# Kernel tuning notes

Hardware: AMD Instinct MI355X
Metric: run time of the kernel (lower is better)

## Reference

```python
import jax, jax.numpy as jnp
import numpy as np

EPS = 1e-8

def setup_inputs() -> dict:
    key = jax.random.key(0)
    k1, k2, k3, k4 = jax.random.split(key, 4)
    B, S, K, N = 8, 32, 8192, 8192
    x = jax.random.normal(k1, (B, S, K), dtype=jnp.float32)
    # unpacked AWQ 4-bit weights: int8 values in [-8, 7] (stored as int32 here)
    qweight = jax.random.randint(k2, (K, N), -8, 8, dtype=jnp.int32)
    w_scales = jax.random.uniform(k3, (N,), dtype=jnp.float32) * 0.01 + 1e-4
    bias = jax.random.normal(k4, (N,), dtype=jnp.float32)
    return {"x": x, "qweight": qweight, "w_scales": w_scales, "bias": bias}

def reference(x, qweight, w_scales, bias):
    K = x.shape[-1]
    x2 = x.reshape(-1, K)                                  # [M, K]
    # per-token symmetric int8 activation quantization
    max_abs = jnp.max(jnp.abs(x2), axis=-1, keepdims=True)  # [M, 1]
    act_scales = jnp.maximum(max_abs / 127.0, EPS)
    x_q = jnp.clip(jnp.round(x2 / act_scales), -127, 127).astype(jnp.int8)
    out = x_q.astype(jnp.float32) @ qweight.astype(jnp.float32)  # [M, N]
    # dequant rescale: per-token * per-channel, then bias
    out = out * act_scales * w_scales[None, :] + bias[None, :]
    out = out.reshape(*x.shape[:-1], out.shape[-1])
    return out.astype(x.dtype)
```

## Files before the change

kernel.cpp:

```cpp
#include <hip/hip_runtime.h>

#define M_ 256
#define K_ 8192
#define N_ 8192

typedef int v4i __attribute__((ext_vector_type(4)));
typedef int v16i __attribute__((ext_vector_type(16)));

__global__ __launch_bounds__(256) void awq_quant(const float* __restrict__ x,
                                                 signed char* __restrict__ xqt,
                                                 float* __restrict__ scales) {
    const int m = blockIdx.x;
    const int t = threadIdx.x;
    const float4* xrow = (const float4*)(x + (size_t)m * K_);
    float4 v[8];
    float mx = 0.0f;
#pragma unroll
    for (int j = 0; j < 8; ++j) {
        v[j] = xrow[j * 256 + t];
        mx = fmaxf(mx, fmaxf(fmaxf(fabsf(v[j].x), fabsf(v[j].y)),
                             fmaxf(fabsf(v[j].z), fabsf(v[j].w))));
    }
#pragma unroll
    for (int off = 32; off > 0; off >>= 1) mx = fmaxf(mx, __shfl_xor(mx, off, 64));
    __shared__ float red[4];
    if ((t & 63) == 0) red[t >> 6] = mx;
    __syncthreads();
    mx = fmaxf(fmaxf(red[0], red[1]), fmaxf(red[2], red[3]));
    const float scale = fmaxf(mx / 127.0f, 1e-8f);

    char* base = (char*)xqt + ((size_t)(m >> 5) << 18);
    const int ml = m & 31;
#pragma unroll
    for (int j = 0; j < 8; ++j) {
        const int q0 = (int)fminf(fmaxf(rintf(v[j].x / scale), -127.0f), 127.0f);
        const int q1 = (int)fminf(fmaxf(rintf(v[j].y / scale), -127.0f), 127.0f);
        const int q2 = (int)fminf(fmaxf(rintf(v[j].z / scale), -127.0f), 127.0f);
        const int q3 = (int)fminf(fmaxf(rintf(v[j].w / scale), -127.0f), 127.0f);
        const int packed = (q0 & 255) | ((q1 & 255) << 8) | ((q2 & 255) << 16) | ((q3 & 255) << 24);
        const int k0 = 4 * (j * 256 + t);
        const int addr = ((k0 >> 8) << 13) + (((k0 >> 5) & 7) << 10) +
                         ((ml + (((k0 >> 4) & 1) << 5)) << 4) + (k0 & 15);
        *(int*)(base + addr) = packed;
    }
    if (t == 0) scales[m] = scale;
}


__device__ __forceinline__ void stage_b(char* btn, int bwo,
                                        const int4& w0, const int4& w1,
                                        const int4& w2, const int4& w3) {
    const int* p0 = (const int*)&w0;
    const int* p1 = (const int*)&w1;
    const int* p2 = (const int*)&w2;
    const int* p3 = (const int*)&w3;
#pragma unroll
    for (int j = 0; j < 4; ++j) {
        const unsigned u = __builtin_amdgcn_perm((unsigned)p1[j], (unsigned)p0[j], 0x00000400u);
        const unsigned w = __builtin_amdgcn_perm((unsigned)p3[j], (unsigned)p2[j], 0x00000400u);
        const unsigned o = __builtin_amdgcn_perm(w, u, 0x05040100u);
        *(unsigned*)(btn + bwo + j * 272) = o;
    }
}

__global__ __launch_bounds__(512) void awq_gemm(const signed char* __restrict__ xqt,
                                                const float* __restrict__ scales,
                                                const int* __restrict__ qw,
                                                const float* __restrict__ wscale,
                                                const float* __restrict__ bias,
                                                float* __restrict__ out) {
    __shared__ __align__(16) char btile[2][32 * 272];
    const int t = threadIdx.x;
    const int lane = t & 63;
    const int wave = t >> 6;
    const int n0 = blockIdx.x * 32;

    const int sa = t & 7;
    const int sr = t >> 3;
    const int* qbase = qw + (size_t)(4 * sr) * N_ + n0 + 4 * sa;

    const signed char* xqb = xqt + ((size_t)wave << 18) + lane * 16;

    const int bro = (lane & 31) * 272 + (lane >> 5) * 16;
    const int bwo = (4 * sa) * 272 + 4 * sr;

    v16i acc = {};
    v4i aF[8];
    int4 sA[4], sB[4];

    auto loadq = [&](int4* dst, int chunk) {
        const int4* q = (const int4*)(qbase + (size_t)chunk * 256 * N_);
        dst[0] = q[0];
        dst[1] = q[N_ / 4];
        dst[2] = q[2 * (N_ / 4)];
        dst[3] = q[3 * (N_ / 4)];
    };

    loadq(sA, 0);
    loadq(sB, 1);
#pragma unroll
    for (int ks = 0; ks < 8; ++ks) aF[ks] = *(const v4i*)(xqb + ks * 1024);
    stage_b(&btile[0][0], bwo, sA[0], sA[1], sA[2], sA[3]);
    asm volatile("s_waitcnt lgkmcnt(0)" ::: "memory");
    __builtin_amdgcn_s_barrier();
    __builtin_amdgcn_sched_barrier(0);

    for (int sc = 0; sc < 32; sc += 2) {
        {
            const int c2 = (sc + 2 < 32) ? sc + 2 : 31;
            loadq(sA, c2);
            const int an = (sc + 1 < 32) ? sc + 1 : 31;
            const char* btc = &btile[0][0];
#pragma unroll
            for (int ks = 0; ks < 8; ++ks) {
                const v4i bf = *(const v4i*)(btc + bro + ks * 32);
                acc = __builtin_amdgcn_mfma_i32_32x32x32_i8(aF[ks], bf, acc, 0, 0, 0);
                aF[ks] = *(const v4i*)(xqb + an * 8192 + ks * 1024);
            }
            stage_b(&btile[1][0], bwo, sB[0], sB[1], sB[2], sB[3]);
            asm volatile("s_waitcnt lgkmcnt(0)" ::: "memory");
            __builtin_amdgcn_s_barrier();
            __builtin_amdgcn_sched_barrier(0);
        }
        {
            const int c3 = (sc + 3 < 32) ? sc + 3 : 31;
            loadq(sB, c3);
            const int an = (sc + 2 < 32) ? sc + 2 : 31;
            const char* btc = &btile[1][0];
#pragma unroll
            for (int ks = 0; ks < 8; ++ks) {
                const v4i bf = *(const v4i*)(btc + bro + ks * 32);
                acc = __builtin_amdgcn_mfma_i32_32x32x32_i8(aF[ks], bf, acc, 0, 0, 0);
                aF[ks] = *(const v4i*)(xqb + an * 8192 + ks * 1024);
            }
            stage_b(&btile[0][0], bwo, sA[0], sA[1], sA[2], sA[3]);
            asm volatile("s_waitcnt lgkmcnt(0)" ::: "memory");
            __builtin_amdgcn_s_barrier();
            __builtin_amdgcn_sched_barrier(0);
        }
    }

    const int n = n0 + (lane & 31);
    const float wn = wscale[n];
    const float bn = bias[n];
    const int mb = wave * 32 + 4 * (lane >> 5);
#pragma unroll
    for (int g = 0; g < 16; ++g) {
        const int m = mb + (g & 3) + 8 * (g >> 2);
        out[(size_t)m * N_ + n] = ((float)acc[g] * scales[m]) * wn + bn;
    }
}

extern "C" void kernel_launch(void* const* d_in, const int* in_sizes, int n_in,
                              void* d_out, int out_size, void* d_ws, size_t ws_size,
                              hipStream_t stream) {
    const float* x    = (const float*)d_in[0];
    const int*   qw   = (const int*)d_in[1];
    const float* wsc  = (const float*)d_in[2];
    const float* bias = (const float*)d_in[3];
    float* out = (float*)d_out;

    signed char* xqbuf  = (signed char*)d_ws;
    float*       scales = (float*)((char*)d_ws + (size_t)M_ * K_);

    awq_quant<<<M_, 256, 0, stream>>>(x, xqbuf, scales);
    awq_gemm<<<N_ / 32, 512, 0, stream>>>(xqbuf, scales, qw, wsc, bias, out);
}
```

Measured before the change: 66.12 us.

## Split GEMM blocks across M halves with 256 threads and 8-row weight staging

Each GEMM block now covers half of the M rows (4 waves) instead of all 256, which doubles the grid to 512 blocks of 256 threads. Each thread therefore loads 8 weight rows per chunk instead of 4 and writes 8-byte LDS stores. Block indices are ordered so that the two M-halves of each group of 8 N-tiles run adjacently, which should help the duplicated weight reads hit in L2. The intent is better occupancy and parallelism across CUs. The cost is that the int32 weights are read twice overall and each thread holds more registers.

```diff
diff --git a/kernel.cpp b/kernel.cpp
--- a/kernel.cpp
+++ b/kernel.cpp
@@ -47,60 +47,58 @@
 }
 
 
-__device__ __forceinline__ void stage_b(char* btn, int bwo,
-                                        const int4& w0, const int4& w1,
-                                        const int4& w2, const int4& w3) {
-    const int* p0 = (const int*)&w0;
-    const int* p1 = (const int*)&w1;
-    const int* p2 = (const int*)&w2;
-    const int* p3 = (const int*)&w3;
+__device__ __forceinline__ void stage_b8(char* btn, int bwo, const int4* w) {
 #pragma unroll
     for (int j = 0; j < 4; ++j) {
-        const unsigned u = __builtin_amdgcn_perm((unsigned)p1[j], (unsigned)p0[j], 0x00000400u);
-        const unsigned w = __builtin_amdgcn_perm((unsigned)p3[j], (unsigned)p2[j], 0x00000400u);
-        const unsigned o = __builtin_amdgcn_perm(w, u, 0x05040100u);
-        *(unsigned*)(btn + bwo + j * 272) = o;
+        const unsigned a0 = __builtin_amdgcn_perm((unsigned)((const int*)&w[1])[j], (unsigned)((const int*)&w[0])[j], 0x00000400u);
+        const unsigned a1 = __builtin_amdgcn_perm((unsigned)((const int*)&w[3])[j], (unsigned)((const int*)&w[2])[j], 0x00000400u);
+        const unsigned b0 = __builtin_amdgcn_perm((unsigned)((const int*)&w[5])[j], (unsigned)((const int*)&w[4])[j], 0x00000400u);
+        const unsigned b1 = __builtin_amdgcn_perm((unsigned)((const int*)&w[7])[j], (unsigned)((const int*)&w[6])[j], 0x00000400u);
+        uint2 o;
+        o.x = __builtin_amdgcn_perm(a1, a0, 0x05040100u);
+        o.y = __builtin_amdgcn_perm(b1, b0, 0x05040100u);
+        *(uint2*)(btn + bwo + j * 272) = o;
     }
 }
 
-__global__ __launch_bounds__(512) void awq_gemm(const signed char* __restrict__ xqt,
-                                                const float* __restrict__ scales,
-                                                const int* __restrict__ qw,
-                                                const float* __restrict__ wscale,
-                                                const float* __restrict__ bias,
-                                                float* __restrict__ out) {
+__global__ __launch_bounds__(256, 2) void awq_gemm(const signed char* __restrict__ xqt,
+                                                   const float* __restrict__ scales,
+                                                   const int* __restrict__ qw,
+                                                   const float* __restrict__ wscale,
+                                                   const float* __restrict__ bias,
+                                                   float* __restrict__ out) {
     __shared__ __align__(16) char btile[2][32 * 272];
     const int t = threadIdx.x;
     const int lane = t & 63;
     const int wave = t >> 6;
-    const int n0 = blockIdx.x * 32;
+    const int bid = blockIdx.x;
+    const int mhalf = (bid >> 3) & 1;
+    const int n0 = ((bid >> 4) * 8 + (bid & 7)) * 32;
 
     const int sa = t & 7;
     const int sr = t >> 3;
-    const int* qbase = qw + (size_t)(4 * sr) * N_ + n0 + 4 * sa;
+    const int* qbase = qw + (size_t)(8 * sr) * N_ + n0 + 4 * sa;
 
-    const signed char* xqb = xqt + ((size_t)wave << 18) + lane * 16;
+    const signed char* xqb = xqt + ((size_t)(mhalf * 4 + wave) << 18) + lane * 16;
 
     const int bro = (lane & 31) * 272 + (lane >> 5) * 16;
-    const int bwo = (4 * sa) * 272 + 4 * sr;
+    const int bwo = (4 * sa) * 272 + 8 * sr;
 
     v16i acc = {};
     v4i aF[8];
-    int4 sA[4], sB[4];
+    int4 sA[8], sB[8];
 
     auto loadq = [&](int4* dst, int chunk) {
         const int4* q = (const int4*)(qbase + (size_t)chunk * 256 * N_);
-        dst[0] = q[0];
-        dst[1] = q[N_ / 4];
-        dst[2] = q[2 * (N_ / 4)];
-        dst[3] = q[3 * (N_ / 4)];
+#pragma unroll
+        for (int i = 0; i < 8; ++i) dst[i] = q[i * (N_ / 4)];
     };
 
     loadq(sA, 0);
     loadq(sB, 1);
 #pragma unroll
     for (int ks = 0; ks < 8; ++ks) aF[ks] = *(const v4i*)(xqb + ks * 1024);
-    stage_b(&btile[0][0], bwo, sA[0], sA[1], sA[2], sA[3]);
+    stage_b8(&btile[0][0], bwo, sA);
     asm volatile("s_waitcnt lgkmcnt(0)" ::: "memory");
     __builtin_amdgcn_s_barrier();
     __builtin_amdgcn_sched_barrier(0);
@@ -117,7 +115,7 @@
                 acc = __builtin_amdgcn_mfma_i32_32x32x32_i8(aF[ks], bf, acc, 0, 0, 0);
                 aF[ks] = *(const v4i*)(xqb + an * 8192 + ks * 1024);
             }
-            stage_b(&btile[1][0], bwo, sB[0], sB[1], sB[2], sB[3]);
+            stage_b8(&btile[1][0], bwo, sB);
             asm volatile("s_waitcnt lgkmcnt(0)" ::: "memory");
             __builtin_amdgcn_s_barrier();
             __builtin_amdgcn_sched_barrier(0);
@@ -133,7 +131,7 @@
                 acc = __builtin_amdgcn_mfma_i32_32x32x32_i8(aF[ks], bf, acc, 0, 0, 0);
                 aF[ks] = *(const v4i*)(xqb + an * 8192 + ks * 1024);
             }
-            stage_b(&btile[0][0], bwo, sA[0], sA[1], sA[2], sA[3]);
+            stage_b8(&btile[0][0], bwo, sA);
             asm volatile("s_waitcnt lgkmcnt(0)" ::: "memory");
             __builtin_amdgcn_s_barrier();
             __builtin_amdgcn_sched_barrier(0);
@@ -143,7 +141,7 @@
     const int n = n0 + (lane & 31);
     const float wn = wscale[n];
     const float bn = bias[n];
-    const int mb = wave * 32 + 4 * (lane >> 5);
+    const int mb = (mhalf * 4 + wave) * 32 + 4 * (lane >> 5);
 #pragma unroll
     for (int g = 0; g < 16; ++g) {
         const int m = mb + (g & 3) + 8 * (g >> 2);
@@ -164,5 +162,5 @@
     float*       scales = (float*)((char*)d_ws + (size_t)M_ * K_);
 
     awq_quant<<<M_, 256, 0, stream>>>(x, xqbuf, scales);
-    awq_gemm<<<N_ / 32, 512, 0, stream>>>(xqbuf, scales, qw, wsc, bias, out);
+    awq_gemm<<<512, 256, 0, stream>>>(xqbuf, scales, qw, wsc, bias, out);
 }
```

Result: slower. 81.34 us (+23.0%).

## Deepen global-load prefetch pipeline to four stages in int8 AWQ GEMM

Applied to the files above, without the earlier changes.

Restructures the GEMM main loop from a two-deep prefetch of weights and activations to a four-deep rotating register pipeline, unrolled by four phases. Each phase issues loads for chunk+4 while computing the current chunk, so more global memory latency can be hidden. Launch bounds also request two blocks per CU, which caps registers even though the extra buffers raise register demand. That combination risks spills or lost occupancy.

```diff
diff --git a/kernel.cpp b/kernel.cpp
--- a/kernel.cpp
+++ b/kernel.cpp
@@ -63,12 +63,12 @@
     }
 }
 
-__global__ __launch_bounds__(512) void awq_gemm(const signed char* __restrict__ xqt,
-                                                const float* __restrict__ scales,
-                                                const int* __restrict__ qw,
-                                                const float* __restrict__ wscale,
-                                                const float* __restrict__ bias,
-                                                float* __restrict__ out) {
+__global__ __launch_bounds__(512, 2) void awq_gemm(const signed char* __restrict__ xqt,
+                                                   const float* __restrict__ scales,
+                                                   const int* __restrict__ qw,
+                                                   const float* __restrict__ wscale,
+                                                   const float* __restrict__ bias,
+                                                   float* __restrict__ out) {
     __shared__ __align__(16) char btile[2][32 * 272];
     const int t = threadIdx.x;
     const int lane = t & 63;
@@ -85,8 +85,8 @@
     const int bwo = (4 * sa) * 272 + 4 * sr;
 
     v16i acc = {};
-    v4i aF[8];
-    int4 sA[4], sB[4];
+    v4i a0[8], a1[8], a2[8], a3[8];
+    int4 s0[4], s1[4], s2[4], s3[4];
 
     auto loadq = [&](int4* dst, int chunk) {
         const int4* q = (const int4*)(qbase + (size_t)chunk * 256 * N_);
@@ -95,50 +95,45 @@
         dst[2] = q[2 * (N_ / 4)];
         dst[3] = q[3 * (N_ / 4)];
     };
+    auto loada = [&](v4i* a, int chunk) {
+#pragma unroll
+        for (int f = 0; f < 8; ++f)
+            a[f] = *(const v4i*)(xqb + (size_t)chunk * 8192 + f * 1024);
+    };
 
-    loadq(sA, 0);
-    loadq(sB, 1);
-#pragma unroll
-    for (int ks = 0; ks < 8; ++ks) aF[ks] = *(const v4i*)(xqb + ks * 1024);
-    stage_b(&btile[0][0], bwo, sA[0], sA[1], sA[2], sA[3]);
+    loadq(s0, 0); loada(a0, 0);
+    loadq(s1, 1); loada(a1, 1);
+    loadq(s2, 2); loada(a2, 2);
+    loadq(s3, 3); loada(a3, 3);
+    stage_b(&btile[0][0], bwo, s0[0], s0[1], s0[2], s0[3]);
     asm volatile("s_waitcnt lgkmcnt(0)" ::: "memory");
     __builtin_amdgcn_s_barrier();
     __builtin_amdgcn_sched_barrier(0);
 
-    for (int sc = 0; sc < 32; sc += 2) {
-        {
-            const int c2 = (sc + 2 < 32) ? sc + 2 : 31;
-            loadq(sA, c2);
-            const int an = (sc + 1 < 32) ? sc + 1 : 31;
-            const char* btc = &btile[0][0];
-#pragma unroll
-            for (int ks = 0; ks < 8; ++ks) {
-                const v4i bf = *(const v4i*)(btc + bro + ks * 32);
-                acc = __builtin_amdgcn_mfma_i32_32x32x32_i8(aF[ks], bf, acc, 0, 0, 0);
-                aF[ks] = *(const v4i*)(xqb + an * 8192 + ks * 1024);
-            }
-            stage_b(&btile[1][0], bwo, sB[0], sB[1], sB[2], sB[3]);
-            asm volatile("s_waitcnt lgkmcnt(0)" ::: "memory");
-            __builtin_amdgcn_s_barrier();
-            __builtin_amdgcn_sched_barrier(0);
-        }
-        {
-            const int c3 = (sc + 3 < 32) ? sc + 3 : 31;
-            loadq(sB, c3);
-            const int an = (sc + 2 < 32) ? sc + 2 : 31;
-            const char* btc = &btile[1][0];
-#pragma unroll
-            for (int ks = 0; ks < 8; ++ks) {
-                const v4i bf = *(const v4i*)(btc + bro + ks * 32);
-                acc = __builtin_amdgcn_mfma_i32_32x32x32_i8(aF[ks], bf, acc, 0, 0, 0);
-                aF[ks] = *(const v4i*)(xqb + an * 8192 + ks * 1024);
-            }
-            stage_b(&btile[0][0], bwo, sA[0], sA[1], sA[2], sA[3]);
-            asm volatile("s_waitcnt lgkmcnt(0)" ::: "memory");
-            __builtin_amdgcn_s_barrier();
-            __builtin_amdgcn_sched_barrier(0);
-        }
+#define PHASE(P_, AREG, SCUR, SNEXT, BUFC, BUFN)                                    \
+    {                                                                               \
+        const int cf = (P_) + 4;                                                    \
+        if (cf < 32) loadq(SCUR, cf);                                               \
+        const char* btc = &btile[BUFC][0];                                          \
+        _Pragma("unroll")                                                           \
+        for (int f = 0; f < 8; ++f) {                                               \
+            const v4i bf = *(const v4i*)(btc + bro + f * 32);                       \
+            acc = __builtin_amdgcn_mfma_i32_32x32x32_i8(AREG[f], bf, acc, 0, 0, 0); \
+        }                                                                           \
+        if (cf < 32) loada(AREG, cf);                                               \
+        stage_b(&btile[BUFN][0], bwo, SNEXT[0], SNEXT[1], SNEXT[2], SNEXT[3]);      \
+        asm volatile("s_waitcnt lgkmcnt(0)" ::: "memory");                          \
+        __builtin_amdgcn_s_barrier();                                               \
+        __builtin_amdgcn_sched_barrier(0);                                          \
     }
+
+    for (int sc = 0; sc < 32; sc += 4) {
+        PHASE(sc + 0, a0, s0, s1, 0, 1)
+        PHASE(sc + 1, a1, s1, s2, 1, 0)
+        PHASE(sc + 2, a2, s2, s3, 0, 1)
+        PHASE(sc + 3, a3, s3, s0, 1, 0)
+    }
+#undef PHASE
 
     const int n = n0 + (lane & 31);
     const float wn = wscale[n];
```

New measurement: 67.60 us. 2.2% more time.
